# Kernel tuning notes

Hardware: AMD Instinct MI355X
Metric: run time of the kernel (lower is better)

The kernel has to match this reference:

```python
import jax, jax.numpy as jnp
import numpy as np

B, N, K, C, CM = 4, 1024, 9, 32, 128
SIGMA = 1.0
EPS = 1e-5
SLOPE = 0.01  # LeakyReLU default negative slope


def _batchnorm(x, gamma, beta):
    # training-mode BatchNorm1d over the point dimension
    m = x.mean(axis=0)
    v = x.var(axis=0)
    return gamma * (x - m) * jax.lax.rsqrt(v + EPS) + beta


def setup_inputs() -> dict:
    key = jax.random.key(0)
    ks = jax.random.split(key, 8)
    positions = jax.random.uniform(ks[0], (B * N, 2), jnp.float32) * 10.0
    weights = jax.random.normal(ks[1], (B * N, C), jnp.float32)
    # learned kernel offsets (grid-init in original; random offsets of same scale here)
    kernel_pos = jax.random.normal(ks[2], (K, 2), jnp.float32) * (2.0 * SIGMA)
    conv_w = jax.random.normal(ks[3], (K, C, C), jnp.float32) / np.sqrt(K * C)
    w1 = jax.random.normal(ks[4], (C, CM), jnp.float32) / np.sqrt(C)
    w2 = jax.random.normal(ks[5], (CM, C), jnp.float32) / np.sqrt(CM)
    return {
        "positions": positions,
        "weights": weights,
        "kernel_pos": kernel_pos,
        "conv_w": conv_w,
        "bn_gamma": jnp.ones((C,), jnp.float32),
        "bn_beta": jnp.zeros((C,), jnp.float32),
        "w1": w1,
        "b1": jnp.zeros((CM,), jnp.float32),
        "bn1_gamma": jnp.ones((CM,), jnp.float32),
        "bn1_beta": jnp.zeros((CM,), jnp.float32),
        "w2": w2,
        "b2": jnp.zeros((C,), jnp.float32),
        "n_batch": B,
        "n_points": N,
    }


def reference(positions, weights, kernel_pos, conv_w, bn_gamma, bn_beta,
              w1, b1, bn1_gamma, bn1_beta, w2, b2, n_batch, n_points):
    b, n = n_batch, n_points
    k = kernel_pos.shape[0]
    c = weights.shape[-1]
    pos = positions.reshape(b, n, 2)
    w = weights.reshape(b, n, c)

    # KernelConv: each component spawns K shifted components with channel mixing
    comp_pos = pos[:, :, None, :] + kernel_pos[None, None, :, :]      # [b,n,k,2]
    comp_w = jnp.einsum('bnc,kcd->bnkd', w, conv_w)                   # [b,n,k,c]

    # KernelSample: evaluate the resulting Gaussian mixture at the input positions
    diff = pos[:, :, None, None, :] - comp_pos[:, None, :, :, :]      # [b,i,n,k,2]
    dist2 = jnp.sum(diff * diff, axis=-1)                             # [b,i,n,k]
    kmat = jnp.exp(-dist2 / (2.0 * SIGMA * SIGMA))
    y = jnp.einsum('bink,bnkc->bic', kmat, comp_w)                    # [b,i,c]
    y = jax.nn.leaky_relu(y, SLOPE)
    y = y.reshape(b * n, c)

    # conv_norm + residual add of input weights
    y = _batchnorm(y, bn_gamma, bn_beta)
    y = y + weights

    # PyG MLP [C, CM, C], act_first=True, plain_last=True
    h = y @ w1 + b1
    h = jax.nn.leaky_relu(h, SLOPE)
    h = _batchnorm(h, bn1_gamma, bn1_beta)
    delta = h @ w2 + b2

    return y + delta  # output weights [b*n, c]; positions pass through unchanged
```

## Files before the change

### kernel.cpp

```cpp
#include <hip/hip_runtime.h>

#define BB 4
#define NN 1024
#define KK 9
#define C  32
#define CM 128
#define M  (BB*NN)
#define EPSB 1e-5f
#define SLOPE 0.01f

#define KPAD 296
#define CHUNK_F16 (32*KPAD)
#define CHUNK_F4  (CHUNK_F16/8)

typedef _Float16 f16x8 __attribute__((ext_vector_type(8)));
typedef _Float16 f16x4 __attribute__((ext_vector_type(4)));
typedef float    f32x4 __attribute__((ext_vector_type(4)));

__device__ __forceinline__ float leaky(float x){ return x > 0.f ? x : SLOPE*x; }

__device__ __forceinline__ float fexp2(float x){
#if __has_builtin(__builtin_amdgcn_exp2f)
  return __builtin_amdgcn_exp2f(x);
#else
  return exp2f(x);
#endif
}

__global__ __launch_bounds__(256) void k1_compw(const float* __restrict__ w,
                                                const float* __restrict__ conv_w,
                                                _Float16* __restrict__ cwh,
                                                float* __restrict__ stats){
  __shared__ float cwl[3*C*C];
  int bid = blockIdx.x;
  int kt  = bid % 3;
  int s   = (bid/3) & 31, b = bid/96;
  int tid = threadIdx.x;
  if (bid == 0){ for (int i = tid; i < 320; i += 256) stats[i] = 0.f; }

  const float4* cs = (const float4*)(conv_w + kt*3*C*C);
  float4* cd = (float4*)cwl;
  for (int v = tid; v < 768; v += 256) cd[v] = cs[v];

  int nl = tid & 31, dq = tid >> 5;
  int row = (b*32 + s)*32 + nl;
  float wreg[32];
  const float4* wr = (const float4*)(w + (size_t)row*C);
  #pragma unroll
  for (int j = 0; j < 8; ++j){
    float4 t = wr[j];
    wreg[4*j]=t.x; wreg[4*j+1]=t.y; wreg[4*j+2]=t.z; wreg[4*j+3]=t.w;
  }
  __syncthreads();

  _Float16* outb = cwh + (size_t)(b*32 + s)*CHUNK_F16;
  const float4* cv = (const float4*)cwl;
  #pragma unroll
  for (int kl = 0; kl < 3; ++kl){
    float a0=0.f, a1=0.f, a2=0.f, a3=0.f;
    #pragma unroll
    for (int c = 0; c < C; ++c){
      float4 t = cv[kl*256 + c*8 + dq];
      a0 += wreg[c]*t.x; a1 += wreg[c]*t.y; a2 += wreg[c]*t.z; a3 += wreg[c]*t.w;
    }
    int k = kt*3 + kl;
    outb[(dq*4+0)*KPAD + k*32 + nl] = (_Float16)a0;
    outb[(dq*4+1)*KPAD + k*32 + nl] = (_Float16)a1;
    outb[(dq*4+2)*KPAD + k*32 + nl] = (_Float16)a2;
    outb[(dq*4+3)*KPAD + k*32 + nl] = (_Float16)a3;
  }
}

__global__ __launch_bounds__(512, 2) void k2_full(const float* __restrict__ pos,
                                                  const float* __restrict__ kpos,
                                                  const _Float16* __restrict__ cwh,
                                                  float* __restrict__ z,
                                                  float* __restrict__ stats){
  __shared__ __align__(16) _Float16 cwt[2][32*KPAD];
  __shared__ __align__(16) _Float16 kmt[2][16*KPAD];
  __shared__ __align__(16) float pnl[NN*2];
  float* red  = (float*)&cwt[0][0];
  float* red2 = (float*)&cwt[1][0];

  int bid = blockIdx.x;
  int b = bid >> 6, it = bid & 63;
  int tid = threadIdx.x;
  int lane = tid & 63, wid = tid >> 6;
  int mm = lane & 15, quad = lane >> 4;
  int c0 = (wid & 1) * 16, q = wid >> 1;
  int ig = tid >> 5, nl = tid & 31;

  const float BETA = -0.72134752f;
  float Ak[KK], Bk[KK], Ck[KK];
  #pragma unroll
  for (int k = 0; k < KK; ++k){
    float kxx = kpos[2*k], kyy = kpos[2*k+1];
    Ak[k] = -2.f*BETA*kxx;
    Bk[k] = -2.f*BETA*kyy;
    Ck[k] = BETA*(kxx*kxx + kyy*kyy);
  }

#define STAGE(dstbuf, ss) do{ \
    const float4* s4_ = (const float4*)(cwh + (size_t)(b*32 + (ss))*CHUNK_F16); \
    _Pragma("unroll") \
    for (int rr_ = 0; rr_ < 3; ++rr_){ \
      int v_ = tid + rr_*512; \
      if (v_ < CHUNK_F4) \
        __builtin_amdgcn_global_load_lds( \
          (const __attribute__((address_space(1))) unsigned int*)(s4_ + v_), \
          (__attribute__((address_space(3))) unsigned int*)((dstbuf) + (size_t)(rr_*512 + wid*64)*8), \
          16, 0, 0); \
    } \
  }while(0)

#define GEN(dstbuf, ss) do{ \
    float dx_ = pix - pnl[2*((ss)*32 + nl)]; \
    float dy_ = piy - pnl[2*((ss)*32 + nl) + 1]; \
    float e0_ = BETA*(dx_*dx_ + dy_*dy_); \
    _Float16* kr_ = (dstbuf) + ig*KPAD + nl; \
    _Pragma("unroll") \
    for (int k = 0; k < KK; ++k){ \
      float t_ = (e0_ + Ck[k]) + dx_*Ak[k] + dy_*Bk[k]; \
      kr_[k*32] = (_Float16)fexp2(t_); \
    } \
  }while(0)

  ((float4*)pnl)[tid] = ((const float4*)(pos + (size_t)b*NN*2))[tid];
  STAGE(cwt[0], 0);
  __syncthreads();
  float pix = pnl[2*(it*16 + ig)];
  float piy = pnl[2*(it*16 + ig) + 1];
  GEN(kmt[0], 0);
  __syncthreads();

  f32x4 acc = {0.f,0.f,0.f,0.f};
  for (int s = 0; s < 32; ++s){
    int cur = s & 1, nxt = cur ^ 1;
    if (s < 31) STAGE(cwt[nxt], s+1);
    #pragma unroll
    for (int t = 0; t < 3; ++t){
      int ks = q + t*4;
      if (ks < KK){
        f16x8 a  = *(const f16x8*)&kmt[cur][mm*KPAD + ks*32 + quad*8];
        f16x8 bf = *(const f16x8*)&cwt[cur][(c0+mm)*KPAD + ks*32 + quad*8];
        acc = __builtin_amdgcn_mfma_f32_16x16x32_f16(a, bf, acc, 0, 0, 0);
      }
    }
    if (s < 31) GEN(kmt[nxt], s+1);
    __syncthreads();
  }
#undef STAGE
#undef GEN

  float* rp = red + wid*256;
  #pragma unroll
  for (int r = 0; r < 4; ++r) rp[(quad*4 + r)*16 + mm] = acc[r];
  __syncthreads();
  {
    int r = tid >> 5, c = tid & 31;
    int half = c >> 4, cc = c & 15;
    int o = r*16 + cc;
    float v = red[half*256 + o] + red[(2+half)*256 + o]
            + red[(4+half)*256 + o] + red[(6+half)*256 + o];
    v = leaky(v);
    z[((size_t)b*NN + it*16 + r)*C + c] = v;
    red2[c*17 + r] = v;
  }
  __syncthreads();
  if (tid < C){
    float s1 = 0.f, s2 = 0.f;
    #pragma unroll
    for (int r = 0; r < 16; ++r){ float t = red2[tid*17 + r]; s1 += t; s2 += t*t; }
    atomicAdd(&stats[tid], s1);
    atomicAdd(&stats[C + tid], s2);
  }
}

__global__ __launch_bounds__(256) void k4_mlp1(const float* __restrict__ z,
                                               const float* __restrict__ weights,
                                               const float* __restrict__ bn_g,
                                               const float* __restrict__ bn_b,
                                               const float* __restrict__ w1,
                                               const float* __restrict__ b1,
                                               float* __restrict__ stats,
                                               float* __restrict__ y,
                                               float* __restrict__ h){
  __shared__ float w1l[C*CM];
  __shared__ float yl[16*C];
  __shared__ float lt1[CM], lt2[CM];
  int tid = threadIdx.x;
  int row0 = blockIdx.x * 16;
  for (int i = tid; i < C*CM; i += 256) w1l[i] = w1[i];
  if (tid < CM){ lt1[tid]=0.f; lt2[tid]=0.f; }
  #pragma unroll
  for (int j = 0; j < 2; ++j){
    int e = tid + j*256;
    int c  = e & (C-1);
    int rl = e >> 5;
    float s1 = stats[c], s2 = stats[C + c];
    float mean = s1 * (1.f/M);
    float var  = s2 * (1.f/M) - mean*mean;
    float sc = bn_g[c] * rsqrtf(var + EPSB);
    float sh = bn_b[c] - mean*sc;
    int row = row0 + rl;
    float v = z[(size_t)row*C + c]*sc + sh + weights[(size_t)row*C + c];
    yl[e] = v;
    y[(size_t)row*C + c] = v;
  }
  __syncthreads();
  #pragma unroll
  for (int j = 0; j < 8; ++j){
    int e = tid + j*256;
    int col = e & (CM-1);
    int rl  = e >> 7;
    float acc = b1[col];
    #pragma unroll
    for (int c = 0; c < C; ++c) acc += yl[rl*C + c] * w1l[c*CM + col];
    acc = leaky(acc);
    h[(size_t)(row0+rl)*CM + col] = acc;
    atomicAdd(&lt1[col], acc);
    atomicAdd(&lt2[col], acc*acc);
  }
  __syncthreads();
  if (tid < CM){
    atomicAdd(&stats[2*C + tid],      lt1[tid]);
    atomicAdd(&stats[2*C + CM + tid], lt2[tid]);
  }
}

__global__ __launch_bounds__(256) void k5_mlp2(const float* __restrict__ h,
                                               const float* __restrict__ y,
                                               const float* __restrict__ bn1_g,
                                               const float* __restrict__ bn1_b,
                                               const float* __restrict__ w2,
                                               const float* __restrict__ b2,
                                               const float* __restrict__ stats,
                                               float* __restrict__ out){
  __shared__ float w2l[CM*C];
  __shared__ float hl[16*CM];
  int tid = threadIdx.x;
  int row0 = blockIdx.x * 16;
  for (int i = tid; i < CM*C; i += 256) w2l[i] = w2[i];
  #pragma unroll
  for (int j = 0; j < 8; ++j){
    int e = tid + j*256;
    int col = e & (CM-1);
    int rl  = e >> 7;
    float t1 = stats[2*C + col], t2 = stats[2*C + CM + col];
    float mean = t1*(1.f/M);
    float var  = t2*(1.f/M) - mean*mean;
    float sc = bn1_g[col]*rsqrtf(var + EPSB);
    float sh = bn1_b[col] - mean*sc;
    hl[e] = h[(size_t)(row0+rl)*CM + col]*sc + sh;
  }
  __syncthreads();
  #pragma unroll
  for (int j = 0; j < 2; ++j){
    int e = tid + j*256;
    int c  = e & (C-1);
    int rl = e >> 5;
    float acc = b2[c];
    #pragma unroll
    for (int jj = 0; jj < CM; ++jj) acc += hl[rl*CM + jj] * w2l[jj*C + c];
    int row = row0 + rl;
    out[(size_t)row*C + c] = y[(size_t)row*C + c] + acc;
  }
}

extern "C" void kernel_launch(void* const* d_in, const int* in_sizes, int n_in,
                              void* d_out, int out_size, void* d_ws, size_t ws_size,
                              hipStream_t stream) {
  const float* positions = (const float*)d_in[0];
  const float* weights   = (const float*)d_in[1];
  const float* kpos      = (const float*)d_in[2];
  const float* conv_w    = (const float*)d_in[3];
  const float* bn_g      = (const float*)d_in[4];
  const float* bn_b      = (const float*)d_in[5];
  const float* w1        = (const float*)d_in[6];
  const float* b1        = (const float*)d_in[7];
  const float* bn1_g     = (const float*)d_in[8];
  const float* bn1_b     = (const float*)d_in[9];
  const float* w2        = (const float*)d_in[10];
  const float* b2        = (const float*)d_in[11];
  float* out = (float*)d_out;

  float* ws = (float*)d_ws;
  size_t off = 0;
  _Float16* cwh = (_Float16*)(ws + off); off += (size_t)128*CHUNK_F16/2;
  float* z     = ws + off; off += (size_t)M*C;
  float* y     = ws + off; off += (size_t)M*C;
  float* h     = ws + off; off += (size_t)M*CM;
  float* stats = ws + off; off += 320;

  k1_compw<<<384, 256, 0, stream>>>(weights, conv_w, cwh, stats);
  k2_full <<<256, 512, 0, stream>>>(positions, kpos, cwh, z, stats);
  k4_mlp1 <<<M/16, 256, 0, stream>>>(z, weights, bn_g, bn_b, w1, b1, stats, y, h);
  k5_mlp2 <<<M/16, 256, 0, stream>>>(h, y, bn1_g, bn1_b, w2, b2, stats, out);
}
```

Before: 144.1 us.

## Fuse all four stages into one cooperative kernel with grid syncs

Merges the component-weight, kernel-sample, MLP1 and MLP2 kernels into a single cooperative launch of 256 blocks, using grid-wide syncs for the batch-norm statistics barriers. Intermediates z, y and h stay in registers and shared memory instead of round-tripping through global memory, and three kernel launch gaps go away. The trade-offs are the cost of grid.sync, only 128 blocks doing the first stage, and a layout that requires all 256 blocks to be co-resident.

```diff
diff --git a/kernel.cpp b/kernel.cpp
--- a/kernel.cpp
+++ b/kernel.cpp
@@ -1,4 +1,7 @@
 #include <hip/hip_runtime.h>
+#include <hip/hip_cooperative_groups.h>
+
+namespace cg = cooperative_groups;
 
 #define BB 4
 #define NN 1024
@@ -14,7 +17,6 @@
 #define CHUNK_F4  (CHUNK_F16/8)
 
 typedef _Float16 f16x8 __attribute__((ext_vector_type(8)));
-typedef _Float16 f16x4 __attribute__((ext_vector_type(4)));
 typedef float    f32x4 __attribute__((ext_vector_type(4)));
 
 __device__ __forceinline__ float leaky(float x){ return x > 0.f ? x : SLOPE*x; }
@@ -27,64 +29,69 @@
 #endif
 }
 
-__global__ __launch_bounds__(256) void k1_compw(const float* __restrict__ w,
-                                                const float* __restrict__ conv_w,
-                                                _Float16* __restrict__ cwh,
-                                                float* __restrict__ stats){
-  __shared__ float cwl[3*C*C];
+__global__ __launch_bounds__(512, 2) void fused_all(
+    const float* __restrict__ pos,
+    const float* __restrict__ wts,
+    const float* __restrict__ kpos,
+    const float* __restrict__ conv_w,
+    const float* __restrict__ bn_g,
+    const float* __restrict__ bn_b,
+    const float* __restrict__ w1,
+    const float* __restrict__ b1,
+    const float* __restrict__ bn1_g,
+    const float* __restrict__ bn1_b,
+    const float* __restrict__ w2,
+    const float* __restrict__ b2,
+    float* __restrict__ out,
+    _Float16* __restrict__ cwh,
+    float* __restrict__ stats)
+{
+  __shared__ __align__(16) char smA[65024];
+  __shared__ float yl[512];
+  __shared__ float lt1[CM], lt2[CM];
+
+  cg::grid_group grid = cg::this_grid();
   int bid = blockIdx.x;
-  int kt  = bid % 3;
-  int s   = (bid/3) & 31, b = bid/96;
   int tid = threadIdx.x;
-  if (bid == 0){ for (int i = tid; i < 320; i += 256) stats[i] = 0.f; }
-
-  const float4* cs = (const float4*)(conv_w + kt*3*C*C);
-  float4* cd = (float4*)cwl;
-  for (int v = tid; v < 768; v += 256) cd[v] = cs[v];
-
-  int nl = tid & 31, dq = tid >> 5;
-  int row = (b*32 + s)*32 + nl;
-  float wreg[32];
-  const float4* wr = (const float4*)(w + (size_t)row*C);
-  #pragma unroll
-  for (int j = 0; j < 8; ++j){
-    float4 t = wr[j];
-    wreg[4*j]=t.x; wreg[4*j+1]=t.y; wreg[4*j+2]=t.z; wreg[4*j+3]=t.w;
-  }
-  __syncthreads();
-
-  _Float16* outb = cwh + (size_t)(b*32 + s)*CHUNK_F16;
-  const float4* cv = (const float4*)cwl;
-  #pragma unroll
-  for (int kl = 0; kl < 3; ++kl){
-    float a0=0.f, a1=0.f, a2=0.f, a3=0.f;
-    #pragma unroll
-    for (int c = 0; c < C; ++c){
-      float4 t = cv[kl*256 + c*8 + dq];
-      a0 += wreg[c]*t.x; a1 += wreg[c]*t.y; a2 += wreg[c]*t.z; a3 += wreg[c]*t.w;
-    }
-    int k = kt*3 + kl;
-    outb[(dq*4+0)*KPAD + k*32 + nl] = (_Float16)a0;
-    outb[(dq*4+1)*KPAD + k*32 + nl] = (_Float16)a1;
-    outb[(dq*4+2)*KPAD + k*32 + nl] = (_Float16)a2;
-    outb[(dq*4+3)*KPAD + k*32 + nl] = (_Float16)a3;
-  }
-}
-
-__global__ __launch_bounds__(512, 2) void k2_full(const float* __restrict__ pos,
-                                                  const float* __restrict__ kpos,
-                                                  const _Float16* __restrict__ cwh,
-                                                  float* __restrict__ z,
-                                                  float* __restrict__ stats){
-  __shared__ __align__(16) _Float16 cwt[2][32*KPAD];
-  __shared__ __align__(16) _Float16 kmt[2][16*KPAD];
-  __shared__ __align__(16) float pnl[NN*2];
-  float* red  = (float*)&cwt[0][0];
-  float* red2 = (float*)&cwt[1][0];
-
-  int bid = blockIdx.x;
+
+  if (bid < 128){
+    float* cwl = (float*)smA;
+    const float4* cs = (const float4*)conv_w;
+    float4* cd = (float4*)cwl;
+    for (int v = tid; v < (KK*C*C)/4; v += 512) cd[v] = cs[v];
+    if (bid == 0){ for (int i = tid; i < 320; i += 512) stats[i] = 0.f; }
+    int nl = tid & 31, dq = tid >> 5;
+    int row = bid*32 + nl;
+    float wreg[32];
+    const float4* wr = (const float4*)(wts + (size_t)row*C);
+    #pragma unroll
+    for (int j = 0; j < 8; ++j){
+      float4 t = wr[j];
+      wreg[4*j]=t.x; wreg[4*j+1]=t.y; wreg[4*j+2]=t.z; wreg[4*j+3]=t.w;
+    }
+    __syncthreads();
+    _Float16* outb = cwh + (size_t)bid*CHUNK_F16;
+    #pragma unroll
+    for (int k = 0; k < KK; ++k){
+      float a0 = 0.f, a1 = 0.f;
+      #pragma unroll
+      for (int c = 0; c < C; ++c){
+        float2 t = *(const float2*)&cwl[k*C*C + c*C + dq*2];
+        a0 += wreg[c]*t.x; a1 += wreg[c]*t.y;
+      }
+      outb[(dq*2+0)*KPAD + k*32 + nl] = (_Float16)a0;
+      outb[(dq*2+1)*KPAD + k*32 + nl] = (_Float16)a1;
+    }
+  }
+  grid.sync();
+
+  _Float16 (*cwt)[32*KPAD] = (_Float16(*)[32*KPAD])smA;
+  _Float16 (*kmt)[16*KPAD] = (_Float16(*)[16*KPAD])(smA + 37888);
+  float* pnl = (float*)(smA + 56832);
+  float* red  = (float*)smA;
+  float* red2 = (float*)(smA + 18944);
+
   int b = bid >> 6, it = bid & 63;
-  int tid = threadIdx.x;
   int lane = tid & 63, wid = tid >> 6;
   int mm = lane & 15, quad = lane >> 4;
   int c0 = (wid & 1) * 16, q = wid >> 1;
@@ -156,15 +163,15 @@
   #pragma unroll
   for (int r = 0; r < 4; ++r) rp[(quad*4 + r)*16 + mm] = acc[r];
   __syncthreads();
+  float zv;
   {
     int r = tid >> 5, c = tid & 31;
     int half = c >> 4, cc = c & 15;
     int o = r*16 + cc;
     float v = red[half*256 + o] + red[(2+half)*256 + o]
             + red[(4+half)*256 + o] + red[(6+half)*256 + o];
-    v = leaky(v);
-    z[((size_t)b*NN + it*16 + r)*C + c] = v;
-    red2[c*17 + r] = v;
+    zv = leaky(v);
+    red2[c*17 + r] = zv;
   }
   __syncthreads();
   if (tid < C){
@@ -174,96 +181,67 @@
     atomicAdd(&stats[tid], s1);
     atomicAdd(&stats[C + tid], s2);
   }
-}
-
-__global__ __launch_bounds__(256) void k4_mlp1(const float* __restrict__ z,
-                                               const float* __restrict__ weights,
-                                               const float* __restrict__ bn_g,
-                                               const float* __restrict__ bn_b,
-                                               const float* __restrict__ w1,
-                                               const float* __restrict__ b1,
-                                               float* __restrict__ stats,
-                                               float* __restrict__ y,
-                                               float* __restrict__ h){
-  __shared__ float w1l[C*CM];
-  __shared__ float yl[16*C];
-  __shared__ float lt1[CM], lt2[CM];
-  int tid = threadIdx.x;
-  int row0 = blockIdx.x * 16;
-  for (int i = tid; i < C*CM; i += 256) w1l[i] = w1[i];
-  if (tid < CM){ lt1[tid]=0.f; lt2[tid]=0.f; }
-  #pragma unroll
-  for (int j = 0; j < 2; ++j){
-    int e = tid + j*256;
-    int c  = e & (C-1);
-    int rl = e >> 5;
+  grid.sync();
+
+  int row0 = bid * 16;
+  float* w1l = (float*)smA;
+  for (int i = tid; i < C*CM; i += 512) w1l[i] = w1[i];
+  if (tid < CM){ lt1[tid] = 0.f; lt2[tid] = 0.f; }
+  {
+    int c = tid & 31, rl = tid >> 5;
     float s1 = stats[c], s2 = stats[C + c];
     float mean = s1 * (1.f/M);
     float var  = s2 * (1.f/M) - mean*mean;
     float sc = bn_g[c] * rsqrtf(var + EPSB);
     float sh = bn_b[c] - mean*sc;
-    int row = row0 + rl;
-    float v = z[(size_t)row*C + c]*sc + sh + weights[(size_t)row*C + c];
-    yl[e] = v;
-    y[(size_t)row*C + c] = v;
-  }
-  __syncthreads();
-  #pragma unroll
-  for (int j = 0; j < 8; ++j){
-    int e = tid + j*256;
-    int col = e & (CM-1);
-    int rl  = e >> 7;
-    float acc = b1[col];
-    #pragma unroll
-    for (int c = 0; c < C; ++c) acc += yl[rl*C + c] * w1l[c*CM + col];
-    acc = leaky(acc);
-    h[(size_t)(row0+rl)*CM + col] = acc;
-    atomicAdd(&lt1[col], acc);
-    atomicAdd(&lt2[col], acc*acc);
+    yl[tid] = zv*sc + sh + wts[(size_t)(row0 + rl)*C + c];
+  }
+  __syncthreads();
+  float hreg[4];
+  {
+    int col = tid & 127;
+    #pragma unroll
+    for (int j = 0; j < 4; ++j){
+      int e = tid + j*512;
+      int rl = e >> 7;
+      float acc1 = b1[col];
+      #pragma unroll
+      for (int c = 0; c < C; ++c) acc1 += yl[rl*C + c] * w1l[c*CM + col];
+      acc1 = leaky(acc1);
+      hreg[j] = acc1;
+      atomicAdd(&lt1[col], acc1);
+      atomicAdd(&lt2[col], acc1*acc1);
+    }
   }
   __syncthreads();
   if (tid < CM){
     atomicAdd(&stats[2*C + tid],      lt1[tid]);
     atomicAdd(&stats[2*C + CM + tid], lt2[tid]);
   }
-}
-
-__global__ __launch_bounds__(256) void k5_mlp2(const float* __restrict__ h,
-                                               const float* __restrict__ y,
-                                               const float* __restrict__ bn1_g,
-                                               const float* __restrict__ bn1_b,
-                                               const float* __restrict__ w2,
-                                               const float* __restrict__ b2,
-                                               const float* __restrict__ stats,
-                                               float* __restrict__ out){
-  __shared__ float w2l[CM*C];
-  __shared__ float hl[16*CM];
-  int tid = threadIdx.x;
-  int row0 = blockIdx.x * 16;
-  for (int i = tid; i < CM*C; i += 256) w2l[i] = w2[i];
-  #pragma unroll
-  for (int j = 0; j < 8; ++j){
-    int e = tid + j*256;
-    int col = e & (CM-1);
-    int rl  = e >> 7;
+  grid.sync();
+
+  float* w2l = (float*)smA;
+  float* hl  = (float*)(smA + 16384);
+  for (int i = tid; i < CM*C; i += 512) w2l[i] = w2[i];
+  {
+    int col = tid & 127;
     float t1 = stats[2*C + col], t2 = stats[2*C + CM + col];
     float mean = t1*(1.f/M);
     float var  = t2*(1.f/M) - mean*mean;
     float sc = bn1_g[col]*rsqrtf(var + EPSB);
     float sh = bn1_b[col] - mean*sc;
-    hl[e] = h[(size_t)(row0+rl)*CM + col]*sc + sh;
-  }
-  __syncthreads();
-  #pragma unroll
-  for (int j = 0; j < 2; ++j){
-    int e = tid + j*256;
-    int c  = e & (C-1);
-    int rl = e >> 5;
-    float acc = b2[c];
-    #pragma unroll
-    for (int jj = 0; jj < CM; ++jj) acc += hl[rl*CM + jj] * w2l[jj*C + c];
-    int row = row0 + rl;
-    out[(size_t)row*C + c] = y[(size_t)row*C + c] + acc;
+    #pragma unroll
+    for (int j = 0; j < 4; ++j){
+      hl[tid + j*512] = hreg[j]*sc + sh;
+    }
+  }
+  __syncthreads();
+  {
+    int c = tid & 31, rl = tid >> 5;
+    float acc2 = b2[c];
+    #pragma unroll
+    for (int jj = 0; jj < CM; ++jj) acc2 += hl[rl*CM + jj] * w2l[jj*C + c];
+    out[(size_t)(row0 + rl)*C + c] = yl[tid] + acc2;
   }
 }
 
@@ -285,15 +263,15 @@
   float* out = (float*)d_out;
 
   float* ws = (float*)d_ws;
-  size_t off = 0;
-  _Float16* cwh = (_Float16*)(ws + off); off += (size_t)128*CHUNK_F16/2;
-  float* z     = ws + off; off += (size_t)M*C;
-  float* y     = ws + off; off += (size_t)M*C;
-  float* h     = ws + off; off += (size_t)M*CM;
-  float* stats = ws + off; off += 320;
-
-  k1_compw<<<384, 256, 0, stream>>>(weights, conv_w, cwh, stats);
-  k2_full <<<256, 512, 0, stream>>>(positions, kpos, cwh, z, stats);
-  k4_mlp1 <<<M/16, 256, 0, stream>>>(z, weights, bn_g, bn_b, w1, b1, stats, y, h);
-  k5_mlp2 <<<M/16, 256, 0, stream>>>(h, y, bn1_g, bn1_b, w2, b2, stats, out);
+  _Float16* cwh = (_Float16*)ws;
+  float* stats  = ws + (size_t)128*CHUNK_F16/2;
+
+  void* args[] = {
+    (void*)&positions, (void*)&weights, (void*)&kpos, (void*)&conv_w,
+    (void*)&bn_g, (void*)&bn_b, (void*)&w1, (void*)&b1,
+    (void*)&bn1_g, (void*)&bn1_b, (void*)&w2, (void*)&b2,
+    (void*)&out, (void*)&cwh, (void*)&stats
+  };
+  hipLaunchCooperativeKernel((void*)fused_all, dim3(256), dim3(512),
+                             args, 0, stream);
 }
```

After: 223.1 us. 54.8% more time.

## Triple-buffer conv weight staging, vectorize kernel-matrix gen, halve MLP block rows

Applied to the files above, without the earlier changes.

The main sample kernel now keeps three LDS buffers for the conv-weight chunks, prefetching two stages ahead. It replaces __syncthreads with explicit vmcnt/lgkmcnt waits and raw barriers so global-to-LDS loads overlap more compute. The Gaussian kernel generation now computes four points per thread and writes packed f16x4 stores, and runs before the MFMAs so it overlaps outstanding loads. The MLP kernels use 8 rows per block, doubling the grid, and accumulate BN stats in registers before the shared atomics. The cost is more LDS per block, lower occupancy risk, and hand-tuned wait counts that must match the number of outstanding loads.

```diff
diff --git a/kernel.cpp b/kernel.cpp
--- a/kernel.cpp
+++ b/kernel.cpp
@@ -71,12 +71,12 @@
   }
 }
 
-__global__ __launch_bounds__(512, 2) void k2_full(const float* __restrict__ pos,
-                                                  const float* __restrict__ kpos,
-                                                  const _Float16* __restrict__ cwh,
-                                                  float* __restrict__ z,
-                                                  float* __restrict__ stats){
-  __shared__ __align__(16) _Float16 cwt[2][32*KPAD];
+__global__ __launch_bounds__(512) void k2_main(const float* __restrict__ pos,
+                                               const float* __restrict__ kpos,
+                                               const _Float16* __restrict__ cwh,
+                                               float* __restrict__ z,
+                                               float* __restrict__ stats){
+  __shared__ __align__(16) _Float16 cwt[3][32*KPAD];
   __shared__ __align__(16) _Float16 kmt[2][16*KPAD];
   __shared__ __align__(16) float pnl[NN*2];
   float* red  = (float*)&cwt[0][0];
@@ -88,7 +88,7 @@
   int lane = tid & 63, wid = tid >> 6;
   int mm = lane & 15, quad = lane >> 4;
   int c0 = (wid & 1) * 16, q = wid >> 1;
-  int ig = tid >> 5, nl = tid & 31;
+  int gk = tid >> 7, ig = (tid >> 3) & 15, np = tid & 7;
 
   const float BETA = -0.72134752f;
   float Ak[KK], Bk[KK], Ck[KK];
@@ -114,43 +114,68 @@
   }while(0)
 
 #define GEN(dstbuf, ss) do{ \
-    float dx_ = pix - pnl[2*((ss)*32 + nl)]; \
-    float dy_ = piy - pnl[2*((ss)*32 + nl) + 1]; \
-    float e0_ = BETA*(dx_*dx_ + dy_*dy_); \
-    _Float16* kr_ = (dstbuf) + ig*KPAD + nl; \
+    float dx_[4], dy_[4], e0_[4]; \
     _Pragma("unroll") \
-    for (int k = 0; k < KK; ++k){ \
-      float t_ = (e0_ + Ck[k]) + dx_*Ak[k] + dy_*Bk[k]; \
-      kr_[k*32] = (_Float16)fexp2(t_); \
+    for (int jj = 0; jj < 4; ++jj){ \
+      int nl_ = np*4 + jj; \
+      dx_[jj] = pix - pnl[2*((ss)*32 + nl_)]; \
+      dy_[jj] = piy - pnl[2*((ss)*32 + nl_) + 1]; \
+      e0_[jj] = BETA*(dx_[jj]*dx_[jj] + dy_[jj]*dy_[jj]); \
+    } \
+    _Pragma("unroll") \
+    for (int t_ = 0; t_ < 3; ++t_){ \
+      int k_ = gk + t_*4; \
+      if (k_ < KK){ \
+        f16x4 ev_; \
+        _Pragma("unroll") \
+        for (int jj = 0; jj < 4; ++jj){ \
+          float x_ = (e0_[jj] + Ck[k_]) + dx_[jj]*Ak[k_] + dy_[jj]*Bk[k_]; \
+          ev_[jj] = (_Float16)fexp2(x_); \
+        } \
+        *(f16x4*)&(dstbuf)[ig*KPAD + k_*32 + np*4] = ev_; \
+      } \
     } \
   }while(0)
 
   ((float4*)pnl)[tid] = ((const float4*)(pos + (size_t)b*NN*2))[tid];
   STAGE(cwt[0], 0);
+  STAGE(cwt[1], 1);
   __syncthreads();
   float pix = pnl[2*(it*16 + ig)];
   float piy = pnl[2*(it*16 + ig) + 1];
   GEN(kmt[0], 0);
-  __syncthreads();
+  asm volatile("s_waitcnt lgkmcnt(0)" ::: "memory");
+  __builtin_amdgcn_s_barrier();
+  __builtin_amdgcn_sched_barrier(0);
 
   f32x4 acc = {0.f,0.f,0.f,0.f};
   for (int s = 0; s < 32; ++s){
-    int cur = s & 1, nxt = cur ^ 1;
-    if (s < 31) STAGE(cwt[nxt], s+1);
+    int cur = s & 1;
+    int ss = (s+2 > 31) ? 31 : s+2;
+    STAGE(cwt[(s+2)%3], ss);
+    if (s < 31) GEN(kmt[cur^1], s+1);
+    asm volatile("s_waitcnt vmcnt(4)" ::: "memory");
+    __builtin_amdgcn_sched_barrier(0);
+    const _Float16* cwb = cwt[s % 3];
     #pragma unroll
     for (int t = 0; t < 3; ++t){
       int ks = q + t*4;
       if (ks < KK){
         f16x8 a  = *(const f16x8*)&kmt[cur][mm*KPAD + ks*32 + quad*8];
-        f16x8 bf = *(const f16x8*)&cwt[cur][(c0+mm)*KPAD + ks*32 + quad*8];
+        f16x8 bf = *(const f16x8*)&cwb[(c0+mm)*KPAD + ks*32 + quad*8];
         acc = __builtin_amdgcn_mfma_f32_16x16x32_f16(a, bf, acc, 0, 0, 0);
       }
     }
-    if (s < 31) GEN(kmt[nxt], s+1);
-    __syncthreads();
+    asm volatile("s_waitcnt lgkmcnt(0)" ::: "memory");
+    __builtin_amdgcn_sched_barrier(0);
+    __builtin_amdgcn_s_barrier();
+    __builtin_amdgcn_sched_barrier(0);
   }
 #undef STAGE
 #undef GEN
+  asm volatile("s_waitcnt vmcnt(0)" ::: "memory");
+  __builtin_amdgcn_s_barrier();
+  __builtin_amdgcn_sched_barrier(0);
 
   float* rp = red + wid*256;
   #pragma unroll
@@ -186,17 +211,15 @@
                                                float* __restrict__ y,
                                                float* __restrict__ h){
   __shared__ float w1l[C*CM];
-  __shared__ float yl[16*C];
+  __shared__ float yl[8*C];
   __shared__ float lt1[CM], lt2[CM];
   int tid = threadIdx.x;
-  int row0 = blockIdx.x * 16;
+  int row0 = blockIdx.x * 8;
   for (int i = tid; i < C*CM; i += 256) w1l[i] = w1[i];
   if (tid < CM){ lt1[tid]=0.f; lt2[tid]=0.f; }
-  #pragma unroll
-  for (int j = 0; j < 2; ++j){
-    int e = tid + j*256;
-    int c  = e & (C-1);
-    int rl = e >> 5;
+  {
+    int c  = tid & (C-1);
+    int rl = tid >> 5;
     float s1 = stats[c], s2 = stats[C + c];
     float mean = s1 * (1.f/M);
     float var  = s2 * (1.f/M) - mean*mean;
@@ -204,22 +227,26 @@
     float sh = bn_b[c] - mean*sc;
     int row = row0 + rl;
     float v = z[(size_t)row*C + c]*sc + sh + weights[(size_t)row*C + c];
-    yl[e] = v;
+    yl[tid] = v;
     y[(size_t)row*C + c] = v;
   }
   __syncthreads();
-  #pragma unroll
-  for (int j = 0; j < 8; ++j){
-    int e = tid + j*256;
-    int col = e & (CM-1);
-    int rl  = e >> 7;
-    float acc = b1[col];
-    #pragma unroll
-    for (int c = 0; c < C; ++c) acc += yl[rl*C + c] * w1l[c*CM + col];
-    acc = leaky(acc);
-    h[(size_t)(row0+rl)*CM + col] = acc;
-    atomicAdd(&lt1[col], acc);
-    atomicAdd(&lt2[col], acc*acc);
+  {
+    int col = tid & (CM-1);
+    float la1 = 0.f, la2 = 0.f;
+    #pragma unroll
+    for (int j = 0; j < 4; ++j){
+      int e = tid + j*256;
+      int rl  = e >> 7;
+      float acc = b1[col];
+      #pragma unroll
+      for (int c = 0; c < C; ++c) acc += yl[rl*C + c] * w1l[c*CM + col];
+      acc = leaky(acc);
+      h[(size_t)(row0+rl)*CM + col] = acc;
+      la1 += acc; la2 += acc*acc;
+    }
+    atomicAdd(&lt1[col], la1);
+    atomicAdd(&lt2[col], la2);
   }
   __syncthreads();
   if (tid < CM){
@@ -237,28 +264,28 @@
                                                const float* __restrict__ stats,
                                                float* __restrict__ out){
   __shared__ float w2l[CM*C];
-  __shared__ float hl[16*CM];
+  __shared__ float hl[8*CM];
   int tid = threadIdx.x;
-  int row0 = blockIdx.x * 16;
+  int row0 = blockIdx.x * 8;
   for (int i = tid; i < CM*C; i += 256) w2l[i] = w2[i];
-  #pragma unroll
-  for (int j = 0; j < 8; ++j){
-    int e = tid + j*256;
-    int col = e & (CM-1);
-    int rl  = e >> 7;
+  {
+    int col = tid & (CM-1);
     float t1 = stats[2*C + col], t2 = stats[2*C + CM + col];
     float mean = t1*(1.f/M);
     float var  = t2*(1.f/M) - mean*mean;
     float sc = bn1_g[col]*rsqrtf(var + EPSB);
     float sh = bn1_b[col] - mean*sc;
-    hl[e] = h[(size_t)(row0+rl)*CM + col]*sc + sh;
-  }
-  __syncthreads();
-  #pragma unroll
-  for (int j = 0; j < 2; ++j){
-    int e = tid + j*256;
-    int c  = e & (C-1);
-    int rl = e >> 5;
+    #pragma unroll
+    for (int j = 0; j < 4; ++j){
+      int e = tid + j*256;
+      int rl  = e >> 7;
+      hl[e] = h[(size_t)(row0+rl)*CM + col]*sc + sh;
+    }
+  }
+  __syncthreads();
+  {
+    int c  = tid & (C-1);
+    int rl = tid >> 5;
     float acc = b2[c];
     #pragma unroll
     for (int jj = 0; jj < CM; ++jj) acc += hl[rl*CM + jj] * w2l[jj*C + c];
@@ -293,7 +320,7 @@
   float* stats = ws + off; off += 320;
 
   k1_compw<<<384, 256, 0, stream>>>(weights, conv_w, cwh, stats);
-  k2_full <<<256, 512, 0, stream>>>(positions, kpos, cwh, z, stats);
-  k4_mlp1 <<<M/16, 256, 0, stream>>>(z, weights, bn_g, bn_b, w1, b1, stats, y, h);
-  k5_mlp2 <<<M/16, 256, 0, stream>>>(h, y, bn1_g, bn1_b, w2, b2, stats, out);
-}
+  k2_main <<<256, 512, 0, stream>>>(positions, kpos, cwh, z, stats);
+  k4_mlp1 <<<M/8, 256, 0, stream>>>(z, weights, bn_g, bn_b, w1, b1, stats, y, h);
+  k5_mlp2 <<<M/8, 256, 0, stream>>>(h, y, bn1_g, bn1_b, w2, b2, stats, out);
+}
```

New measurement: 139.2 us. -3.4%, faster.
